# Performance work log

Measured on AMD Instinct MI355X. Metric: run time of the kernel, lower is better.

Reference implementation:

```python
import jax, jax.numpy as jnp
import numpy as np

N, IN_DIM, OUT_DIM, H = 50000, 128, 128, 4
C = OUT_DIM // H  # 32, per-head channels
E = 1_600_000
NEG_SLOPE = 0.2
LN_EPS = 1e-5


def setup_inputs() -> dict:
    key = jax.random.key(0)
    ks = jax.random.split(key, 12)
    x = jax.random.normal(ks[0], (N, IN_DIM), dtype=jnp.float32)
    edge_index = jax.random.randint(ks[1], (2, E), 0, N, dtype=jnp.int64)
    edge_weight = jax.random.uniform(ks[2], (E,), dtype=jnp.float32)
    s = 1.0 / np.sqrt(IN_DIM)
    W = jax.random.normal(ks[3], (IN_DIM, H * C), dtype=jnp.float32) * s
    att_src = jax.random.normal(ks[4], (1, H, C), dtype=jnp.float32) * s
    att_dst = jax.random.normal(ks[5], (1, H, C), dtype=jnp.float32) * s
    W_edge = jax.random.normal(ks[6], (1, H * C), dtype=jnp.float32)
    att_edge = jax.random.normal(ks[7], (1, H, C), dtype=jnp.float32) * s
    bias = jnp.zeros((H * C,), dtype=jnp.float32)
    ln_gamma = jnp.ones((OUT_DIM,), dtype=jnp.float32)
    ln_beta = jnp.zeros((OUT_DIM,), dtype=jnp.float32)
    return {"x": x, "edge_index": edge_index, "edge_weight": edge_weight,
            "W": W, "att_src": att_src, "att_dst": att_dst,
            "W_edge": W_edge, "att_edge": att_edge, "bias": bias,
            "ln_gamma": ln_gamma, "ln_beta": ln_beta}


def _gat_forward(x, edge_index, edge_weight, W, att_src, att_dst, W_edge, att_edge, bias):
    # GATConv(in, C, heads=H, edge_dim=1), concat=True, add_self_loops=True (fill_value='mean')
    xp = (x @ W).reshape(N, H, C)                      # [N,H,C]
    a_src = jnp.sum(xp * att_src, axis=-1)             # [N,H]
    a_dst = jnp.sum(xp * att_dst, axis=-1)             # [N,H]

    # add self-loops; self-loop edge_attr = mean of existing edge_attr
    loop = jnp.arange(N, dtype=edge_index.dtype)
    src = jnp.concatenate([edge_index[0], loop])       # [E+N]
    dst = jnp.concatenate([edge_index[1], loop])
    ew = jnp.concatenate([edge_weight, jnp.full((N,), jnp.mean(edge_weight), edge_weight.dtype)])

    ea = (ew[:, None] @ W_edge).reshape(-1, H, C)      # [E+N,H,C]
    a_edge = jnp.sum(ea * att_edge, axis=-1)           # [E+N,H]

    logits = a_src[src] + a_dst[dst] + a_edge          # [E+N,H]
    logits = jax.nn.leaky_relu(logits, NEG_SLOPE)

    # segment softmax over destination-node neighborhoods
    m = jax.ops.segment_max(logits, dst, num_segments=N)     # [N,H]
    ex = jnp.exp(logits - m[dst])
    denom = jax.ops.segment_sum(ex, dst, num_segments=N)     # [N,H]
    attn = ex / (denom[dst] + 1e-16)                          # [E+N,H]

    msg = attn[:, :, None] * xp[src]                          # [E+N,H,C]
    out = jax.ops.segment_sum(msg, dst, num_segments=N)      # [N,H,C]
    return out.reshape(N, H * C) + bias


def reference(x, edge_index, edge_weight, W, att_src, att_dst, W_edge, att_edge, bias, ln_gamma, ln_beta):
    out = _gat_forward(x, edge_index, edge_weight, W, att_src, att_dst, W_edge, att_edge, bias)
    # LayerNorm
    mu = jnp.mean(out, axis=-1, keepdims=True)
    var = jnp.mean(jnp.square(out - mu), axis=-1, keepdims=True)
    out = (out - mu) / jnp.sqrt(var + LN_EPS) * ln_gamma + ln_beta
    # ELU (dropout is identity in eval)
    return jax.nn.elu(out)
```

## Files before the change

### kernel.cpp

```cpp
#include <hip/hip_runtime.h>
#include <hip/hip_fp16.h>
#include <cstddef>

#define N_NODES 50000
#define E_EDGES 1600000
#define NEG_SLOPE 0.2f
#define LN_EPS 1e-5f
#define LOG2E 1.4426950408889634f
#define PAD 96

#define NBK 196
#define BCAP 10240
#define PCH 4096
#define NCH 391
#define NGB 1563
#define TPB 256

#define OFF_SCAL    0u
#define OFF_BCUR    256u
#define OFF_EWPART  2048u
#define OFF_COUNTS  8192u
#define OFF_ASRC    208256u
#define OFF_ADST    1008256u
#define OFF_XPH     1808256u
#define OFF_PAIRS   14608256u
#define OFF_STAGE   33808256u

__device__ __forceinline__ float lrelu(float x) { return x > 0.f ? x : NEG_SLOPE * x; }

__device__ __forceinline__ float sel4(float4 v, int h) {
    float ab = (h & 1) ? v.y : v.x;
    float cd = (h & 1) ? v.w : v.z;
    return (h & 2) ? cd : ab;
}

__device__ __forceinline__ float4 fma4(float s, float4 a, float4 c) {
    c.x = fmaf(s, a.x, c.x); c.y = fmaf(s, a.y, c.y);
    c.z = fmaf(s, a.z, c.z); c.w = fmaf(s, a.w, c.w);
    return c;
}

__global__ __launch_bounds__(256, 5) void k_A(const float* __restrict__ x, const float* __restrict__ W,
                                              const float* __restrict__ att_src, const float* __restrict__ att_dst,
                                              const float* __restrict__ W_edge, const float* __restrict__ att_edge,
                                              const int* __restrict__ ei, const float* __restrict__ ew,
                                              unsigned short* __restrict__ xph, float* __restrict__ a_src,
                                              float* __restrict__ a_dst, float* __restrict__ scal,
                                              int* __restrict__ bcur, uint2* __restrict__ staging,
                                              float* __restrict__ ewPart) {
    __shared__ float sx[32 * 128];
    __shared__ float sW[32 * 128];
    int t = threadIdx.x;

    if (blockIdx.x < NCH) {
        int* cnt   = (int*)sx;
        int* gbase = cnt + NBK;
        float* wred = (float*)(gbase + NBK);
        for (int i = t; i < NBK; i += 256) cnt[i] = 0;
        __syncthreads();

        int e0 = blockIdx.x * PCH;
        int lr[16];
        float s_ew = 0.f;
        #pragma unroll
        for (int i = 0; i < 16; i++) {
            int e = e0 + i * 256 + t;
            lr[i] = 0;
            if (e < E_EDGES) {
                int d = ei[E_EDGES + e];
                s_ew += ew[e];
                lr[i] = atomicAdd(&cnt[d >> 8], 1);
            }
        }
        #pragma unroll
        for (int off = 32; off; off >>= 1) s_ew += __shfl_down(s_ew, off, 64);
        if ((t & 63) == 0) wred[t >> 6] = s_ew;
        __syncthreads();
        if (t == 0) ewPart[blockIdx.x] = wred[0] + wred[1] + wred[2] + wred[3];
        for (int i = t; i < NBK; i += 256) gbase[i] = atomicAdd(&bcur[i], cnt[i]);
        __syncthreads();

        #pragma unroll
        for (int i = 0; i < 16; i++) {
            int e = e0 + i * 256 + t;
            if (e < E_EDGES) {
                int s = ei[e];
                int d = ei[E_EDGES + e];
                float w = ew[e];
                int b = d >> 8;
                uint2 ent;
                ent.x = (unsigned int)s |
                        ((unsigned int)__half_as_ushort(__float2half_rn(w)) << 16);
                ent.y = (unsigned int)d;
                staging[(size_t)b * BCAP + gbase[b] + lr[i]] = ent;
            }
        }
        return;
    }

    int gb = blockIdx.x - NCH;
    if (gb == 0 && t < 128) {
        float p = W_edge[t] * att_edge[t];
        #pragma unroll
        for (int off = 16; off; off >>= 1) p += __shfl_down(p, off, 32);
        if ((t & 31) == 0) scal[4 + (t >> 5)] = p;
    }
    int r0 = gb * 32;
    int tc = t & 31;
    int tr = t >> 5;

    for (int i = t; i < 1024; i += 256) {
        int row = i >> 5;
        float4 v = make_float4(0.f, 0.f, 0.f, 0.f);
        if (r0 + row < N_NODES) v = ((const float4*)x)[(size_t)(r0 + row) * 32 + (i & 31)];
        ((float4*)sx)[i] = v;
    }

    float4 acc[4];
    #pragma unroll
    for (int r = 0; r < 4; r++) acc[r] = make_float4(0.f, 0.f, 0.f, 0.f);

    for (int kc = 0; kc < 128; kc += 32) {
        __syncthreads();
        for (int i = t; i < 1024; i += 256)
            ((float4*)sW)[i] = ((const float4*)W)[(size_t)kc * 32 + i];
        __syncthreads();
        #pragma unroll 4
        for (int k4 = 0; k4 < 8; k4++) {
            float4 w0 = ((float4*)sW)[(k4 * 4 + 0) * 32 + tc];
            float4 w1 = ((float4*)sW)[(k4 * 4 + 1) * 32 + tc];
            float4 w2 = ((float4*)sW)[(k4 * 4 + 2) * 32 + tc];
            float4 w3 = ((float4*)sW)[(k4 * 4 + 3) * 32 + tc];
            #pragma unroll
            for (int r = 0; r < 4; r++) {
                float4 xv = ((float4*)sx)[(tr * 4 + r) * 32 + (kc >> 2) + k4];
                acc[r] = fma4(xv.x, w0, acc[r]);
                acc[r] = fma4(xv.y, w1, acc[r]);
                acc[r] = fma4(xv.z, w2, acc[r]);
                acc[r] = fma4(xv.w, w3, acc[r]);
            }
        }
    }

    float4 s4 = ((const float4*)att_src)[tc];
    float4 d4 = ((const float4*)att_dst)[tc];
    int h = tc >> 3;
    #pragma unroll
    for (int r = 0; r < 4; r++) {
        int row = r0 + tr * 4 + r;
        if (row < N_NODES) {
            __half2 h01 = __floats2half2_rn(acc[r].x, acc[r].y);
            __half2 h23 = __floats2half2_rn(acc[r].z, acc[r].w);
            uint2 pk;
            pk.x = *(unsigned int*)&h01;
            pk.y = *(unsigned int*)&h23;
            ((uint2*)xph)[(size_t)row * 32 + tc] = pk;
            float ps = acc[r].x * s4.x + acc[r].y * s4.y + acc[r].z * s4.z + acc[r].w * s4.w;
            float pd = acc[r].x * d4.x + acc[r].y * d4.y + acc[r].z * d4.z + acc[r].w * d4.w;
            ps += __shfl_down(ps, 4, 8); ps += __shfl_down(ps, 2, 8); ps += __shfl_down(ps, 1, 8);
            pd += __shfl_down(pd, 4, 8); pd += __shfl_down(pd, 2, 8); pd += __shfl_down(pd, 1, 8);
            if ((tc & 7) == 0) {
                a_src[(size_t)row * 4 + h] = ps;
                a_dst[(size_t)row * 4 + h] = pd;
            }
        }
    }
}

__global__ __launch_bounds__(256) void k_p2(const uint2* __restrict__ staging,
                                            const int* __restrict__ bcur,
                                            const float* __restrict__ ewPart,
                                            unsigned int* __restrict__ pairs,
                                            int* __restrict__ counts, float* __restrict__ scal) {
    int b = blockIdx.x, t = threadIdx.x;
    __shared__ int cnt2[256];
    __shared__ float wr2[4];
    if (b == 0) {
        float s = 0.f;
        for (int i = t; i < NCH; i += 256) s += ewPart[i];
        #pragma unroll
        for (int off = 32; off; off >>= 1) s += __shfl_down(s, off, 64);
        if ((t & 63) == 0) wr2[t >> 6] = s;
    }
    cnt2[t] = 0;
    __syncthreads();
    if (b == 0 && t == 0) scal[0] = wr2[0] + wr2[1] + wr2[2] + wr2[3];
    int tot = bcur[b];
    const uint2* sg = staging + (size_t)b * BCAP;
    for (int i = t; i < tot; i += 256) {
        uint2 ent = sg[i];
        int d = (int)ent.y;
        int r = atomicAdd(&cnt2[d & 255], 1);
        pairs[(size_t)d * PAD + r] = ent.x;
    }
    __syncthreads();
    int n = (b << 8) + t;
    if (n < N_NODES) counts[n] = cnt2[t];
}

__global__ __launch_bounds__(256) void k_p3(const unsigned int* __restrict__ xpu,
                                            const float* __restrict__ a_src,
                                            const float* __restrict__ a_dst,
                                            const int* __restrict__ counts,
                                            const unsigned int* __restrict__ pairs,
                                            const float* __restrict__ scal,
                                            const float* __restrict__ bias,
                                            const float* __restrict__ gamma,
                                            const float* __restrict__ beta,
                                            float* __restrict__ out) {
    int lane = threadIdx.x & 63;
    int wid = blockIdx.x * 4 + (threadIdx.x >> 6);
    int h = lane >> 4;
    int em = lane & 15;
    int shb = lane & 48;
    float4 K = *(const float4*)(scal + 4);
    float Kh = sel4(K, h);
    float mean_ew = scal[0] * (1.0f / E_EDGES);

    int n = wid;
    if (n >= N_NODES) return;
    {
        int cnt = counts[n];
        float4 ad4 = *(const float4*)(a_dst + (size_t)4 * n);
        float4 as4 = *(const float4*)(a_src + (size_t)4 * n);
        float adh = sel4(ad4, h);
        float aself = exp2f(lrelu(sel4(as4, h) + adh + Kh * mean_ew) * LOG2E);

        unsigned int pv = xpu[(size_t)n * 64 + lane];
        float2 f = __half22float2(*(__half2*)&pv);
        float acc0 = aself * f.x, acc1 = aself * f.y;
        float den = 0.f;

        for (int base = 0; base < cnt; base += 16) {
            int e = base + em;
            float alpha = 0.f;
            int s = n;
            if (e < cnt) {
                unsigned int pk = pairs[(size_t)n * PAD + e];
                s = (int)(pk & 0xFFFFu);
                float w = __half2float(__ushort_as_half((unsigned short)(pk >> 16)));
                float4 av = *(const float4*)(a_src + (size_t)4 * s);
                alpha = exp2f(lrelu(sel4(av, h) + adh + Kh * w) * LOG2E);
            }
            den += alpha;
            #pragma unroll
            for (int j = 0; j < 16; j++) {
                int sj   = __shfl(s, shb + j, 64);
                float aj = __shfl(alpha, shb + j, 64);
                unsigned int p2 = xpu[(size_t)sj * 64 + lane];
                float2 g = __half22float2(*(__half2*)&p2);
                acc0 = fmaf(aj, g.x, acc0);
                acc1 = fmaf(aj, g.y, acc1);
            }
        }
        den += __shfl_xor(den, 1, 64);
        den += __shfl_xor(den, 2, 64);
        den += __shfl_xor(den, 4, 64);
        den += __shfl_xor(den, 8, 64);
        den += aself;

        float inv = 1.0f / (den + 1e-16f);
        float2 b2 = ((const float2*)bias)[lane];
        float y0 = fmaf(acc0, inv, b2.x);
        float y1 = fmaf(acc1, inv, b2.y);

        float s1 = y0 + y1;
        #pragma unroll
        for (int off = 1; off < 64; off <<= 1) s1 += __shfl_xor(s1, off, 64);
        float mu = s1 * (1.f / 128.f);
        float d0 = y0 - mu, d1 = y1 - mu;
        float s2 = d0 * d0 + d1 * d1;
        #pragma unroll
        for (int off = 1; off < 64; off <<= 1) s2 += __shfl_xor(s2, off, 64);
        float rstd = rsqrtf(s2 * (1.f / 128.f) + LN_EPS);
        float2 g2 = ((const float2*)gamma)[lane];
        float2 be2 = ((const float2*)beta)[lane];
        float o0 = fmaf(d0 * rstd, g2.x, be2.x);
        float o1 = fmaf(d1 * rstd, g2.y, be2.y);
        o0 = o0 > 0.f ? o0 : expm1f(o0);
        o1 = o1 > 0.f ? o1 : expm1f(o1);
        float2 o; o.x = o0; o.y = o1;
        ((float2*)out)[(size_t)n * 64 + lane] = o;
    }
}

extern "C" void kernel_launch(void* const* d_in, const int* in_sizes, int n_in,
                              void* d_out, int out_size, void* d_ws, size_t ws_size,
                              hipStream_t stream) {
    const float* x        = (const float*)d_in[0];
    const int*   ei       = (const int*)d_in[1];
    const float* ew       = (const float*)d_in[2];
    const float* W        = (const float*)d_in[3];
    const float* att_src  = (const float*)d_in[4];
    const float* att_dst  = (const float*)d_in[5];
    const float* W_edge   = (const float*)d_in[6];
    const float* att_edge = (const float*)d_in[7];
    const float* bias     = (const float*)d_in[8];
    const float* gamma    = (const float*)d_in[9];
    const float* beta     = (const float*)d_in[10];
    float* out = (float*)d_out;

    char* ws = (char*)d_ws;
    float* scal      = (float*)(ws + OFF_SCAL);
    int*   bcur      = (int*)(ws + OFF_BCUR);
    float* ewPart    = (float*)(ws + OFF_EWPART);
    int*   counts    = (int*)(ws + OFF_COUNTS);
    float* a_src     = (float*)(ws + OFF_ASRC);
    float* a_dst     = (float*)(ws + OFF_ADST);
    unsigned short* xph = (unsigned short*)(ws + OFF_XPH);
    unsigned int* pairs = (unsigned int*)(ws + OFF_PAIRS);
    uint2* staging   = (uint2*)(ws + OFF_STAGE);

    hipMemsetAsync(bcur, 0, NBK * sizeof(int), stream);
    k_A<<<NCH + NGB, TPB, 0, stream>>>(x, W, att_src, att_dst, W_edge, att_edge, ei, ew,
                                       xph, a_src, a_dst, scal, bcur, staging, ewPart);
    k_p2<<<NBK, TPB, 0, stream>>>(staging, bcur, ewPart, pairs, counts, scal);
    k_p3<<<12500, TPB, 0, stream>>>((const unsigned int*)xph, a_src, a_dst, counts, pairs, scal,
                                    bias, gamma, beta, out);
}
```

Baseline: 214.4 us.

## Gather neighbor rows with 16-byte loads across four edges per wave

The aggregation kernel now has each group of 16 lanes load a full 256-byte fp16 feature row with uint4 loads, so one wave fetches four neighbor rows per step instead of one row per step with 4-byte loads. Each lane accumulates eight channels, and the partial sums from the four lane groups are combined with cross-lane shuffles. LayerNorm then works on the 16-lane groups, and only the first group writes the output. This cuts gather instructions and loop trips in exchange for more registers, extra shuffle reductions and redundant LayerNorm work in three idle groups.

```diff
diff --git a/kernel.cpp b/kernel.cpp
--- a/kernel.cpp
+++ b/kernel.cpp
@@ -198,7 +198,7 @@
     if (n < N_NODES) counts[n] = cnt2[t];
 }
 
-__global__ __launch_bounds__(256) void k_p3(const unsigned int* __restrict__ xpu,
+__global__ __launch_bounds__(256) void k_p3(const uint4* __restrict__ xp4,
                                             const float* __restrict__ a_src,
                                             const float* __restrict__ a_dst,
                                             const int* __restrict__ counts,
@@ -209,78 +209,123 @@
                                             const float* __restrict__ beta,
                                             float* __restrict__ out) {
     int lane = threadIdx.x & 63;
-    int wid = blockIdx.x * 4 + (threadIdx.x >> 6);
-    int h = lane >> 4;
+    int n = blockIdx.x * 4 + (threadIdx.x >> 6);
+    if (n >= N_NODES) return;
+
+    int h  = lane >> 4;
     int em = lane & 15;
-    int shb = lane & 48;
+    int L  = lane & 15;
+    int hc = L >> 2;
+
     float4 K = *(const float4*)(scal + 4);
     float Kh = sel4(K, h);
     float mean_ew = scal[0] * (1.0f / E_EDGES);
 
-    int n = wid;
-    if (n >= N_NODES) return;
-    {
-        int cnt = counts[n];
-        float4 ad4 = *(const float4*)(a_dst + (size_t)4 * n);
-        float4 as4 = *(const float4*)(a_src + (size_t)4 * n);
-        float adh = sel4(ad4, h);
-        float aself = exp2f(lrelu(sel4(as4, h) + adh + Kh * mean_ew) * LOG2E);
-
-        unsigned int pv = xpu[(size_t)n * 64 + lane];
-        float2 f = __half22float2(*(__half2*)&pv);
-        float acc0 = aself * f.x, acc1 = aself * f.y;
-        float den = 0.f;
-
-        for (int base = 0; base < cnt; base += 16) {
-            int e = base + em;
-            float alpha = 0.f;
-            int s = n;
-            if (e < cnt) {
-                unsigned int pk = pairs[(size_t)n * PAD + e];
-                s = (int)(pk & 0xFFFFu);
-                float w = __half2float(__ushort_as_half((unsigned short)(pk >> 16)));
-                float4 av = *(const float4*)(a_src + (size_t)4 * s);
-                alpha = exp2f(lrelu(sel4(av, h) + adh + Kh * w) * LOG2E);
-            }
-            den += alpha;
+    int cnt = counts[n];
+    float4 ad4 = *(const float4*)(a_dst + (size_t)4 * n);
+    float4 as4 = *(const float4*)(a_src + (size_t)4 * n);
+    float adh = sel4(ad4, h);
+    float aself = exp2f(lrelu(sel4(as4, h) + adh + Kh * mean_ew) * LOG2E);
+    uint4 pself = *(const uint4*)((const char*)xp4 + (((unsigned)n) << 8) + (L << 4));
+
+    float acc[8];
+    #pragma unroll
+    for (int k = 0; k < 8; k++) acc[k] = 0.f;
+    float den = 0.f;
+
+    for (int base = 0; base < cnt; base += 16) {
+        int e = base + em;
+        float alpha = 0.f;
+        int s = n;
+        if (e < cnt) {
+            unsigned int pk = pairs[(size_t)n * PAD + e];
+            s = (int)(pk & 0xFFFFu);
+            float w = __half2float(__ushort_as_half((unsigned short)(pk >> 16)));
+            float4 av = *(const float4*)(a_src + (size_t)4 * s);
+            alpha = exp2f(lrelu(sel4(av, h) + adh + Kh * w) * LOG2E);
+        }
+        den += alpha;
+        #pragma unroll
+        for (int j = 0; j < 4; j++) {
+            int m = j * 4 + h;
+            int sj   = __shfl(s, m, 64);
+            float aj = __shfl(alpha, (hc << 4) + m, 64);
+            uint4 p = *(const uint4*)((const char*)xp4 + (((unsigned)sj) << 8) + (L << 4));
+            const __half2* hp = (const __half2*)&p;
             #pragma unroll
-            for (int j = 0; j < 16; j++) {
-                int sj   = __shfl(s, shb + j, 64);
-                float aj = __shfl(alpha, shb + j, 64);
-                unsigned int p2 = xpu[(size_t)sj * 64 + lane];
-                float2 g = __half22float2(*(__half2*)&p2);
-                acc0 = fmaf(aj, g.x, acc0);
-                acc1 = fmaf(aj, g.y, acc1);
-            }
-        }
-        den += __shfl_xor(den, 1, 64);
-        den += __shfl_xor(den, 2, 64);
-        den += __shfl_xor(den, 4, 64);
-        den += __shfl_xor(den, 8, 64);
-        den += aself;
-
-        float inv = 1.0f / (den + 1e-16f);
-        float2 b2 = ((const float2*)bias)[lane];
-        float y0 = fmaf(acc0, inv, b2.x);
-        float y1 = fmaf(acc1, inv, b2.y);
-
-        float s1 = y0 + y1;
-        #pragma unroll
-        for (int off = 1; off < 64; off <<= 1) s1 += __shfl_xor(s1, off, 64);
-        float mu = s1 * (1.f / 128.f);
-        float d0 = y0 - mu, d1 = y1 - mu;
-        float s2 = d0 * d0 + d1 * d1;
-        #pragma unroll
-        for (int off = 1; off < 64; off <<= 1) s2 += __shfl_xor(s2, off, 64);
-        float rstd = rsqrtf(s2 * (1.f / 128.f) + LN_EPS);
-        float2 g2 = ((const float2*)gamma)[lane];
-        float2 be2 = ((const float2*)beta)[lane];
-        float o0 = fmaf(d0 * rstd, g2.x, be2.x);
-        float o1 = fmaf(d1 * rstd, g2.y, be2.y);
-        o0 = o0 > 0.f ? o0 : expm1f(o0);
-        o1 = o1 > 0.f ? o1 : expm1f(o1);
-        float2 o; o.x = o0; o.y = o1;
-        ((float2*)out)[(size_t)n * 64 + lane] = o;
+            for (int k = 0; k < 4; k++) {
+                float2 g = __half22float2(hp[k]);
+                acc[2 * k]     = fmaf(aj, g.x, acc[2 * k]);
+                acc[2 * k + 1] = fmaf(aj, g.y, acc[2 * k + 1]);
+            }
+        }
+    }
+
+    #pragma unroll
+    for (int k = 0; k < 8; k++) {
+        acc[k] += __shfl_xor(acc[k], 16, 64);
+        acc[k] += __shfl_xor(acc[k], 32, 64);
+    }
+
+    den += __shfl_xor(den, 1, 64);
+    den += __shfl_xor(den, 2, 64);
+    den += __shfl_xor(den, 4, 64);
+    den += __shfl_xor(den, 8, 64);
+    den += aself;
+
+    float denc   = __shfl(den,   hc << 4, 64);
+    float aselfc = __shfl(aself, hc << 4, 64);
+
+    const __half2* hs = (const __half2*)&pself;
+    #pragma unroll
+    for (int k = 0; k < 4; k++) {
+        float2 g = __half22float2(hs[k]);
+        acc[2 * k]     = fmaf(aselfc, g.x, acc[2 * k]);
+        acc[2 * k + 1] = fmaf(aselfc, g.y, acc[2 * k + 1]);
+    }
+
+    float inv = 1.0f / (denc + 1e-16f);
+    float4 b0 = ((const float4*)bias)[2 * L];
+    float4 b1 = ((const float4*)bias)[2 * L + 1];
+    float y[8];
+    y[0] = fmaf(acc[0], inv, b0.x); y[1] = fmaf(acc[1], inv, b0.y);
+    y[2] = fmaf(acc[2], inv, b0.z); y[3] = fmaf(acc[3], inv, b0.w);
+    y[4] = fmaf(acc[4], inv, b1.x); y[5] = fmaf(acc[5], inv, b1.y);
+    y[6] = fmaf(acc[6], inv, b1.z); y[7] = fmaf(acc[7], inv, b1.w);
+
+    float s1 = 0.f;
+    #pragma unroll
+    for (int k = 0; k < 8; k++) s1 += y[k];
+    s1 += __shfl_xor(s1, 1, 64);
+    s1 += __shfl_xor(s1, 2, 64);
+    s1 += __shfl_xor(s1, 4, 64);
+    s1 += __shfl_xor(s1, 8, 64);
+    float mu = s1 * (1.f / 128.f);
+    float s2 = 0.f;
+    #pragma unroll
+    for (int k = 0; k < 8; k++) { y[k] -= mu; s2 += y[k] * y[k]; }
+    s2 += __shfl_xor(s2, 1, 64);
+    s2 += __shfl_xor(s2, 2, 64);
+    s2 += __shfl_xor(s2, 4, 64);
+    s2 += __shfl_xor(s2, 8, 64);
+    float rstd = rsqrtf(s2 * (1.f / 128.f) + LN_EPS);
+
+    if (h == 0) {
+        float4 g0 = ((const float4*)gamma)[2 * L];
+        float4 g1 = ((const float4*)gamma)[2 * L + 1];
+        float4 e0 = ((const float4*)beta)[2 * L];
+        float4 e1 = ((const float4*)beta)[2 * L + 1];
+        float gg[8] = {g0.x, g0.y, g0.z, g0.w, g1.x, g1.y, g1.z, g1.w};
+        float ee[8] = {e0.x, e0.y, e0.z, e0.w, e1.x, e1.y, e1.z, e1.w};
+        float o[8];
+        #pragma unroll
+        for (int k = 0; k < 8; k++) {
+            float v = fmaf(y[k] * rstd, gg[k], ee[k]);
+            o[k] = v > 0.f ? v : expm1f(v);
+        }
+        float4* op = (float4*)(out + (size_t)n * 128 + 8 * L);
+        op[0] = make_float4(o[0], o[1], o[2], o[3]);
+        op[1] = make_float4(o[4], o[5], o[6], o[7]);
     }
 }
 
@@ -315,6 +360,6 @@
     k_A<<<NCH + NGB, TPB, 0, stream>>>(x, W, att_src, att_dst, W_edge, att_edge, ei, ew,
                                        xph, a_src, a_dst, scal, bcur, staging, ewPart);
     k_p2<<<NBK, TPB, 0, stream>>>(staging, bcur, ewPart, pairs, counts, scal);
-    k_p3<<<12500, TPB, 0, stream>>>((const unsigned int*)xph, a_src, a_dst, counts, pairs, scal,
+    k_p3<<<12500, TPB, 0, stream>>>((const uint4*)xph, a_src, a_dst, counts, pairs, scal,
                                     bias, gamma, beta, out);
 }
```

New measurement: 223.2 us. +4.1%, slower.
